# Optimization experiments

Hardware: AMD Instinct MI355X
Metric: run time of the kernel (lower is better)

## Reference

```python
import jax, jax.numpy as jnp
import numpy as np

D = 1024
H = 16
DH = D // H
FF = 4096
EPS = 1e-5


def _layernorm(x, g, b):
    m = jnp.mean(x, axis=-1, keepdims=True)
    v = jnp.mean(jnp.square(x - m), axis=-1, keepdims=True)
    return (x - m) * jax.lax.rsqrt(v + EPS) * g + b


def setup_inputs() -> dict:
    key = jax.random.key(0)
    ks = jax.random.split(key, 24)
    B, S = 2, 2048
    s = 0.02
    inp = {
        "tokens": jax.random.normal(ks[0], (B, S, D), jnp.float32),
        "attention_bias": jax.random.normal(ks[1], (B, S, S, 3), jnp.float32),
        "metadata_compatibility": jax.random.normal(ks[2], (B, S, S), jnp.float32),
        "key_padding_mask": jnp.zeros((B, S), jnp.bool_),
        "ln1_g": jnp.ones((D,), jnp.float32),
        "ln1_b": jnp.zeros((D,), jnp.float32),
        "Wq": jax.random.normal(ks[3], (D, D), jnp.float32) * s,
        "bq": jnp.zeros((D,), jnp.float32),
        "Wk": jax.random.normal(ks[4], (D, D), jnp.float32) * s,
        "bk": jnp.zeros((D,), jnp.float32),
        "Wv": jax.random.normal(ks[5], (D, D), jnp.float32) * s,
        "bv": jnp.zeros((D,), jnp.float32),
        "Wo": jax.random.normal(ks[6], (D, D), jnp.float32) * s,
        "bo": jnp.zeros((D,), jnp.float32),
        "Ws": jax.random.normal(ks[7], (3, H), jnp.float32) * s,
        "bs": jnp.zeros((H,), jnp.float32),
        "Wm": jax.random.normal(ks[8], (1, H), jnp.float32) * s,
        "bm": jnp.zeros((H,), jnp.float32),
        "ln2_g": jnp.ones((D,), jnp.float32),
        "ln2_b": jnp.zeros((D,), jnp.float32),
        "W1": jax.random.normal(ks[9], (D, FF), jnp.float32) * s,
        "b1": jnp.zeros((FF,), jnp.float32),
        "W2": jax.random.normal(ks[10], (FF, D), jnp.float32) * s,
        "b2": jnp.zeros((D,), jnp.float32),
    }
    return inp


def reference(tokens, attention_bias, metadata_compatibility, key_padding_mask,
              ln1_g, ln1_b, Wq, bq, Wk, bk, Wv, bv, Wo, bo,
              Ws, bs, Wm, bm, ln2_g, ln2_b, W1, b1, W2, b2):
    B, S, _ = tokens.shape
    scale = DH ** -0.5
    n = _layernorm(tokens, ln1_g, ln1_b)
    # project and split heads: [B,S,H,DH]
    q = (n @ Wq + bq).reshape(B, S, H, DH)
    k = (n @ Wk + bk).reshape(B, S, H, DH)
    v = (n @ Wv + bv).reshape(B, S, H, DH)
    logits = jnp.einsum('bihd,bjhd->bhij', q, k) * scale  # [B,H,S,S]
    # structural bias: Linear(3->H) then permute to [B,H,S,S]
    logits = logits + jnp.einsum('bijc,ch->bhij', attention_bias, Ws) + bs[None, :, None, None]
    # metadata bias: Linear(1->H)
    logits = logits + metadata_compatibility[:, None, :, :] * Wm[0][None, :, None, None] + bm[None, :, None, None]
    logits = jnp.where(key_padding_mask[:, None, None, :], -1e9, logits)
    w = jax.nn.softmax(logits, axis=-1)
    attended = jnp.einsum('bhij,bjhd->bihd', w, v).reshape(B, S, D)
    x = tokens + (attended @ Wo + bo)
    h = _layernorm(x, ln2_g, ln2_b)
    ff = jax.nn.gelu(h @ W1 + b1, approximate=False) @ W2 + b2
    return x + ff
```

## Files before the change

kernel.cpp:

```cpp
#include <hip/hip_runtime.h>

#define S_LEN 2048
#define DMODEL 1024
#define NH 16
#define DH 64
#define FFDIM 4096

typedef __bf16 bf16x8 __attribute__((ext_vector_type(8)));
typedef float f32x4 __attribute__((ext_vector_type(4)));
typedef unsigned short ushort_t;

#define AS1 __attribute__((address_space(1)))
#define AS3 __attribute__((address_space(3)))

__device__ __forceinline__ void gll16(const void* g, void* l) {
  __builtin_amdgcn_global_load_lds((AS1 const void*)g, (AS3 void*)l, 16, 0, 0);
}

__device__ __forceinline__ unsigned short f2b(float f){
  unsigned u = __builtin_bit_cast(unsigned, f);
  u = (u + 0x7FFFu + ((u >> 16) & 1u)) >> 16;
  return (unsigned short)u;
}

__device__ __forceinline__ float b2f(unsigned short us){
  return __builtin_bit_cast(float, (unsigned)us << 16);
}

__device__ __forceinline__ unsigned cvt_pk_bf16(float lo, float hi){
  unsigned r;
  asm("v_cvt_pk_bf16_f32 %0, %1, %2" : "=v"(r) : "v"(lo), "v"(hi));
  return r;
}

__device__ __forceinline__ float gelu_exact(float x){
  return 0.5f * x * (1.0f + erff(x * 0.70710678118654752f));
}

__device__ __forceinline__ f32x4 mfma16(bf16x8 a, bf16x8 b, f32x4 c){
  return __builtin_amdgcn_mfma_f32_16x16x32_bf16(a, b, c, 0, 0, 0);
}

__global__ __launch_bounds__(256) void tconv64(
    const float* __restrict__ s0, const float* __restrict__ s1,
    const float* __restrict__ s2, const float* __restrict__ s3,
    const float* __restrict__ s4, const float* __restrict__ s5,
    ushort_t* __restrict__ d0, ushort_t* __restrict__ d1,
    ushort_t* __restrict__ d2, ushort_t* __restrict__ d3,
    ushort_t* __restrict__ d4, ushort_t* __restrict__ d5)
{
  __shared__ float tile[64][65];
  int bx = blockIdx.x;
  const float* W; ushort_t* Wt; int K, N, n0, k0;
  if (bx < 1024) {
    int seg = bx >> 8, t_ = bx & 255;
    W  = (seg == 0) ? s0 : (seg == 1) ? s1 : (seg == 2) ? s2 : s3;
    Wt = (seg == 0) ? d0 : (seg == 1) ? d1 : (seg == 2) ? d2 : d3;
    K = 1024; N = 1024; n0 = (t_ & 15) * 64; k0 = (t_ >> 4) * 64;
  } else if (bx < 2048) {
    int t_ = bx - 1024;
    W = s4; Wt = d4; K = 1024; N = 4096;
    n0 = (t_ & 63) * 64; k0 = (t_ >> 6) * 64;
  } else {
    int t_ = bx - 2048;
    W = s5; Wt = d5; K = 4096; N = 1024;
    n0 = (t_ & 15) * 64; k0 = (t_ >> 4) * 64;
  }
  int t = threadIdx.x;
  int lrow = t >> 4, lcol = (t & 15) * 4;
#pragma unroll
  for (int i = 0; i < 4; ++i) {
    float4 v = *(const float4*)&W[(size_t)(k0 + lrow + i * 16) * N + n0 + lcol];
    tile[lrow + i * 16][lcol]     = v.x;
    tile[lrow + i * 16][lcol + 1] = v.y;
    tile[lrow + i * 16][lcol + 2] = v.z;
    tile[lrow + i * 16][lcol + 3] = v.w;
  }
  __syncthreads();
  int orow = t >> 2, oseg = (t & 3) * 16;
  alignas(16) ushort_t ob[16];
#pragma unroll
  for (int j = 0; j < 16; ++j) ob[j] = f2b(tile[oseg + j][orow]);
  *(uint4*)&Wt[(size_t)(n0 + orow) * K + k0 + oseg]     = *(const uint4*)ob;
  *(uint4*)&Wt[(size_t)(n0 + orow) * K + k0 + oseg + 8] = *((const uint4*)ob + 1);
}

__global__ __launch_bounds__(256) void ln_kernel(
    const float* __restrict__ x, const float* __restrict__ g,
    const float* __restrict__ bt, ushort_t* __restrict__ out)
{
  int row = blockIdx.x;
  int t = threadIdx.x;
  const float4 v = *(const float4*)&x[(size_t)row * DMODEL + t * 4];
  float s = v.x + v.y + v.z + v.w;
  float s2 = v.x*v.x + v.y*v.y + v.z*v.z + v.w*v.w;
#pragma unroll
  for (int d = 1; d < 64; d <<= 1) {
    s  += __shfl_xor(s,  d, 64);
    s2 += __shfl_xor(s2, d, 64);
  }
  __shared__ float red[8];
  int w = t >> 6;
  if ((t & 63) == 0) { red[w] = s; red[4 + w] = s2; }
  __syncthreads();
  s  = red[0] + red[1] + red[2] + red[3];
  s2 = red[4] + red[5] + red[6] + red[7];
  float mean = s * (1.0f / DMODEL);
  float var  = s2 * (1.0f / DMODEL) - mean * mean;
  float rstd = rsqrtf(var + 1e-5f);
  float4 gg = *(const float4*)&g[t * 4];
  float4 bb = *(const float4*)&bt[t * 4];
  ushort4 o;
  o.x = f2b((v.x - mean) * rstd * gg.x + bb.x);
  o.y = f2b((v.y - mean) * rstd * gg.y + bb.y);
  o.z = f2b((v.z - mean) * rstd * gg.z + bb.z);
  o.w = f2b((v.w - mean) * rstd * gg.w + bb.w);
  *(ushort4*)&out[(size_t)row * DMODEL + t * 4] = o;
}

__global__ __launch_bounds__(256) void bias_head_kernel(
    const float* __restrict__ ab, const float* __restrict__ mc,
    const unsigned char* __restrict__ kp,
    const float* __restrict__ Ws, const float* __restrict__ bs,
    const float* __restrict__ Wm, const float* __restrict__ bm,
    ushort_t* __restrict__ bp)
{
  int bi = blockIdx.x;
  int b = bi >> 11;
  int t = threadIdx.x;
  int j0 = t * 8;
  float av[24];
  const float4* A4 = (const float4*)(ab + ((size_t)bi * S_LEN + j0) * 3);
#pragma unroll
  for (int u = 0; u < 6; ++u) {
    float4 x = A4[u];
    av[u*4] = x.x; av[u*4+1] = x.y; av[u*4+2] = x.z; av[u*4+3] = x.w;
  }
  float mv[8];
  const float4* M4 = (const float4*)(mc + (size_t)bi * S_LEN + j0);
#pragma unroll
  for (int u = 0; u < 2; ++u) {
    float4 x = M4[u];
    mv[u*4] = x.x; mv[u*4+1] = x.y; mv[u*4+2] = x.z; mv[u*4+3] = x.w;
  }
  unsigned long long kq = *(const unsigned long long*)(kp + (size_t)b * S_LEN + j0);
#pragma unroll
  for (int h = 0; h < NH; ++h) {
    float w0 = Ws[h], w1 = Ws[NH + h], w2 = Ws[2*NH + h];
    float wm = Wm[h], cc = bs[h] + bm[h];
    float v[8];
#pragma unroll
    for (int j = 0; j < 8; ++j) {
      float vv = av[j*3]*w0 + av[j*3+1]*w1 + av[j*3+2]*w2 + mv[j]*wm + cc;
      if ((kq >> (8*j)) & 1ull) vv = -1e9f;
      v[j] = vv;
    }
    uint4 pk;
    pk.x = cvt_pk_bf16(v[0], v[1]);
    pk.y = cvt_pk_bf16(v[2], v[3]);
    pk.z = cvt_pk_bf16(v[4], v[5]);
    pk.w = cvt_pk_bf16(v[6], v[7]);
    *(uint4*)&bp[((size_t)(b*NH + h) * S_LEN + (bi & (S_LEN-1))) * S_LEN + j0] = pk;
  }
}

template<int MODE>
__global__ __launch_bounds__(256) void gemm_bt(
    const ushort_t* __restrict__ A, const ushort_t* __restrict__ Bt,
    const float* __restrict__ b0p, const float* __restrict__ b1p,
    const float* __restrict__ b2p,
    void* __restrict__ o0, void* __restrict__ o1, void* __restrict__ o2,
    int M, int N, int K)
{
  __shared__ ushort_t sh[2][8192];
  int t = threadIdx.x;
  int m0 = blockIdx.y * 128, n0 = blockIdx.x * 128;
  int w = t >> 6, l = t & 63, lr = l & 15, lg = l >> 4;
  int wr = (w >> 1) * 64, wc = (w & 1) * 64;

  const ushort_t* srcp[4];
  int dsto[4];
#pragma unroll
  for (int j = 0; j < 4; ++j) {
    int c = j * 4 + w;
    int o = c * 1024 + l * 16;
    if (c < 8)
      srcp[j] = &A[(size_t)(m0 + (o >> 6)) * K + ((o & 63) >> 1)];
    else {
      int o2 = o - 8192;
      srcp[j] = &Bt[(size_t)(n0 + (o2 >> 6)) * K + ((o2 & 63) >> 1)];
    }
    dsto[j] = o;
  }

#define GSTAGE(bi, kk) do { \
  _Pragma("unroll") \
  for (int j = 0; j < 4; ++j) gll16(srcp[j] + (kk), (char*)sh[bi] + dsto[j]); \
} while (0)

  GSTAGE(0, 0);
  __syncthreads();
  f32x4 acc[4][4] = {};
  int cur = 0;
  for (int k0 = 0; k0 < K; k0 += 32) {
    if (k0 + 32 < K) GSTAGE(cur ^ 1, k0 + 32);
    const ushort_t* s = sh[cur];
    bf16x8 af[4], bfr[4];
#pragma unroll
    for (int a = 0; a < 4; ++a)
      af[a] = *(const bf16x8*)&s[(wr + a * 16 + lr) * 32 + lg * 8];
#pragma unroll
    for (int b = 0; b < 4; ++b)
      bfr[b] = *(const bf16x8*)&s[4096 + (wc + b * 16 + lr) * 32 + lg * 8];
    __builtin_amdgcn_s_setprio(1);
#pragma unroll
    for (int a = 0; a < 4; ++a)
#pragma unroll
      for (int b = 0; b < 4; ++b)
        acc[a][b] = mfma16(af[a], bfr[b], acc[a][b]);
    __builtin_amdgcn_s_setprio(0);
    __syncthreads();
    cur ^= 1;
  }
#undef GSTAGE

  if (MODE == 3) {
    ushort_t* out = (ushort_t*)o0;
#pragma unroll
    for (int a = 0; a < 4; ++a)
#pragma unroll
      for (int b = 0; b < 4; ++b) {
        int gn = n0 + wc + b * 16 + lr;
        float bv = b0p[gn];
#pragma unroll
        for (int r = 0; r < 4; ++r) {
          int gm = m0 + wr + a * 16 + lg * 4 + r;
          out[(size_t)gm * N + gn] = f2b(gelu_exact(acc[a][b][r] + bv));
        }
      }
  } else {
    int seg = n0 >> 10;
    int nb0 = n0 & 1023;
    const float* bi = (seg == 0) ? b0p : (seg == 1) ? b1p : b2p;
    if (seg < 2) {
      ushort_t* out = (ushort_t*)((seg == 0) ? o0 : o1);
#pragma unroll
      for (int a = 0; a < 4; ++a)
#pragma unroll
        for (int b = 0; b < 4; ++b) {
          int nn = nb0 + wc + b * 16 + lr;
          float bv = bi[nn];
#pragma unroll
          for (int r = 0; r < 4; ++r) {
            int gm = m0 + wr + a * 16 + lg * 4 + r;
            out[(size_t)gm * DMODEL + nn] = f2b(acc[a][b][r] + bv);
          }
        }
    } else {
      ushort_t* out = (ushort_t*)o2;
#pragma unroll
      for (int a = 0; a < 4; ++a)
#pragma unroll
        for (int b = 0; b < 4; ++b) {
          int nn = nb0 + wc + b * 16 + lr;
          int gm = m0 + wr + a * 16 + lg * 4;
          float bv = bi[nn];
          ushort4 pk;
          pk.x = f2b(acc[a][b][0] + bv);
          pk.y = f2b(acc[a][b][1] + bv);
          pk.z = f2b(acc[a][b][2] + bv);
          pk.w = f2b(acc[a][b][3] + bv);
          size_t addr = (((size_t)(gm >> 11) * NH + (nn >> 6)) * DH + (nn & 63)) * S_LEN
                        + (gm & (S_LEN - 1));
          *(ushort4*)&out[addr] = pk;
        }
    }
  }
}

__global__ __launch_bounds__(256) void gemm64_res(
    const ushort_t* __restrict__ A, const ushort_t* __restrict__ Bt,
    const float* __restrict__ bias, const float* __restrict__ res,
    float* __restrict__ out, int M, int N, int K)
{
  __shared__ ushort_t sh[2][6144];
  int t = threadIdx.x;
  int m0 = blockIdx.y * 128, n0 = blockIdx.x * 64;
  int w = t >> 6, l = t & 63, lr = l & 15, lg = l >> 4;
  int wr = (w >> 1) * 64, wc = (w & 1) * 32;

  const ushort_t* srcp[3];
  int dsto[3];
#pragma unroll
  for (int j = 0; j < 3; ++j) {
    int c = j * 4 + w;
    int o = c * 1024 + l * 16;
    if (c < 8)
      srcp[j] = &A[(size_t)(m0 + (o >> 6)) * K + ((o & 63) >> 1)];
    else {
      int o2 = o - 8192;
      srcp[j] = &Bt[(size_t)(n0 + (o2 >> 6)) * K + ((o2 & 63) >> 1)];
    }
    dsto[j] = o;
  }

#define GSTAGE64(bi, kk) do { \
  _Pragma("unroll") \
  for (int j = 0; j < 3; ++j) gll16(srcp[j] + (kk), (char*)sh[bi] + dsto[j]); \
} while (0)

  GSTAGE64(0, 0);
  __syncthreads();
  f32x4 acc[4][2] = {};
  int cur = 0;
  for (int k0 = 0; k0 < K; k0 += 32) {
    if (k0 + 32 < K) GSTAGE64(cur ^ 1, k0 + 32);
    const ushort_t* s = sh[cur];
    bf16x8 af[4], bfr[2];
#pragma unroll
    for (int a = 0; a < 4; ++a)
      af[a] = *(const bf16x8*)&s[(wr + a * 16 + lr) * 32 + lg * 8];
#pragma unroll
    for (int b = 0; b < 2; ++b)
      bfr[b] = *(const bf16x8*)&s[4096 + (wc + b * 16 + lr) * 32 + lg * 8];
    __builtin_amdgcn_s_setprio(1);
#pragma unroll
    for (int a = 0; a < 4; ++a)
#pragma unroll
      for (int b = 0; b < 2; ++b)
        acc[a][b] = mfma16(af[a], bfr[b], acc[a][b]);
    __builtin_amdgcn_s_setprio(0);
    __syncthreads();
    cur ^= 1;
  }
#undef GSTAGE64

#pragma unroll
  for (int a = 0; a < 4; ++a)
#pragma unroll
    for (int b = 0; b < 2; ++b) {
      int gn = n0 + wc + b * 16 + lr;
      float bv = bias[gn];
#pragma unroll
      for (int r = 0; r < 4; ++r) {
        int gm = m0 + wr + a * 16 + lg * 4 + r;
        out[(size_t)gm * N + gn] = acc[a][b][r] + bv + res[(size_t)gm * N + gn];
      }
    }
}

__global__ __launch_bounds__(256) void attn_kernel(
    const ushort_t* __restrict__ q, const ushort_t* __restrict__ k,
    const ushort_t* __restrict__ vt, const ushort_t* __restrict__ bp,
    ushort_t* __restrict__ att)
{
  __shared__ ushort_t kbuf[2][4096];
  __shared__ ushort_t vbuf[2][4096];
  __shared__ ushort_t p_lds[4096];
  int bh = blockIdx.y;
  int b = bh >> 4, h = bh & 15;
  int i0 = blockIdx.x * 64;
  int t = threadIdx.x, w = t >> 6, l = t & 63;
  int lr = l & 15, lg = l >> 4;
  int rho = lr & 7;
  const float scale = 0.125f;
  const int NT = S_LEN / 64;

  int srow0 = t >> 3, srow1 = 32 + (t >> 3);
  int c16 = t & 7;
  size_t kb0 = (size_t)b * S_LEN * DMODEL + h * DH;
  size_t vb0 = (size_t)(b * NH + h) * DH * S_LEN;
  size_t koff0 = (size_t)srow0 * DMODEL + ((c16 ^ (srow0 & 7)) << 3);
  size_t koff1 = (size_t)srow1 * DMODEL + ((c16 ^ (srow1 & 7)) << 3);
  size_t voff0 = (size_t)srow0 * S_LEN + ((c16 ^ (srow0 & 7)) << 3);
  size_t voff1 = (size_t)srow1 * S_LEN + ((c16 ^ (srow1 & 7)) << 3);
  int do0 = t * 8, do1 = 2048 + t * 8;

#define STAGE_KV(bi, j0_) do { \
  size_t kr = kb0 + (size_t)(j0_) * DMODEL; \
  size_t vr = vb0 + (size_t)(j0_); \
  gll16(k + kr + koff0, &kbuf[bi][do0]); \
  gll16(k + kr + koff1, &kbuf[bi][do1]); \
  gll16(vt + vr + voff0, &vbuf[bi][do0]); \
  gll16(vt + vr + voff1, &vbuf[bi][do1]); \
} while (0)

  int qrow = i0 + w * 16 + lr;
  size_t qbase = (size_t)(b * S_LEN + qrow) * DMODEL + h * DH;
  bf16x8 aq0 = *(const bf16x8*)&q[qbase + lg * 8];
  bf16x8 aq1 = *(const bf16x8*)&q[qbase + 32 + lg * 8];

  const ushort_t* bprow = bp + ((size_t)bh * S_LEN + qrow) * S_LEN + lg * 4;

  f32x4 acc_o[4] = {};
  float m_run = -1e30f, l_run = 0.0f;

  uint2 braw[4];
#pragma unroll
  for (int n = 0; n < 4; ++n) braw[n] = *(const uint2*)(bprow + n * 16);

  STAGE_KV(0, 0);
  __syncthreads();

  for (int jt = 0; jt < NT; ++jt) {
    int cur = jt & 1;
    if (jt + 1 < NT) STAGE_KV(cur ^ 1, (jt + 1) * 64);

    uint2 bn[4] = {braw[0], braw[1], braw[2], braw[3]};
    if (jt + 1 < NT) {
      const ushort_t* bpt = bprow + (jt + 1) * 64;
#pragma unroll
      for (int n = 0; n < 4; ++n) bn[n] = *(const uint2*)(bpt + n * 16);
    }

    const char* kbc = (const char*)kbuf[cur];
    f32x4 acc_s[4] = {};
    __builtin_amdgcn_s_setprio(1);
#pragma unroll
    for (int n = 0; n < 4; ++n) {
      const char* rb = kbc + (n * 16 + lr) * 128;
      bf16x8 k0 = *(const bf16x8*)(rb + ((lg ^ rho) << 4));
      bf16x8 k1 = *(const bf16x8*)(rb + (((4 + lg) ^ rho) << 4));
      acc_s[n] = mfma16(k0, aq0, acc_s[n]);
      acc_s[n] = mfma16(k1, aq1, acc_s[n]);
    }
    __builtin_amdgcn_s_setprio(0);

    float p[16];
#pragma unroll
    for (int n = 0; n < 4; ++n) {
      p[n*4+0] = fmaf(acc_s[n][0], scale, b2f((unsigned short)(braw[n].x & 0xFFFF)));
      p[n*4+1] = fmaf(acc_s[n][1], scale, b2f((unsigned short)(braw[n].x >> 16)));
      p[n*4+2] = fmaf(acc_s[n][2], scale, b2f((unsigned short)(braw[n].y & 0xFFFF)));
      p[n*4+3] = fmaf(acc_s[n][3], scale, b2f((unsigned short)(braw[n].y >> 16)));
    }
    float t8[8], t4[4];
#pragma unroll
    for (int i = 0; i < 8; ++i) t8[i] = fmaxf(p[i], p[i + 8]);
#pragma unroll
    for (int i = 0; i < 4; ++i) t4[i] = fmaxf(t8[i], t8[i + 4]);
    float mx = fmaxf(fmaxf(t4[0], t4[1]), fmaxf(t4[2], t4[3]));
    mx = fmaxf(mx, __shfl_xor(mx, 16, 64));
    mx = fmaxf(mx, __shfl_xor(mx, 32, 64));

    if (!__all(mx <= m_run + 8.0f)) {
      float mnew = fmaxf(m_run, mx);
      float sf = __expf(m_run - mnew);
      m_run = mnew;
      l_run *= sf;
      float sfr[4];
#pragma unroll
      for (int r = 0; r < 4; ++r) sfr[r] = __shfl(sf, lg * 4 + r, 64);
#pragma unroll
      for (int nd = 0; nd < 4; ++nd)
#pragma unroll
        for (int r = 0; r < 4; ++r) acc_o[nd][r] *= sfr[r];
    }
#pragma unroll
    for (int i = 0; i < 16; ++i) p[i] = __expf(p[i] - m_run);
    float s8[8], s4[4];
#pragma unroll
    for (int i = 0; i < 8; ++i) s8[i] = p[i] + p[i + 8];
#pragma unroll
    for (int i = 0; i < 4; ++i) s4[i] = s8[i] + s8[i + 4];
    float ls = (s4[0] + s4[1]) + (s4[2] + s4[3]);
    ls += __shfl_xor(ls, 16, 64);
    ls += __shfl_xor(ls, 32, 64);
    l_run += ls;

    char* pb = (char*)p_lds + (w * 16 + lr) * 128;
#pragma unroll
    for (int n = 0; n < 4; ++n) {
      uint2 pk2;
      pk2.x = cvt_pk_bf16(p[n*4+0], p[n*4+1]);
      pk2.y = cvt_pk_bf16(p[n*4+2], p[n*4+3]);
      *(uint2*)(pb + ((n * 32 + lg * 8) ^ (rho << 4))) = pk2;
    }
    asm volatile("s_waitcnt lgkmcnt(0)" ::: "memory");
    __builtin_amdgcn_sched_barrier(0);

    bf16x8 ap0 = *(const bf16x8*)(pb + ((lg ^ rho) << 4));
    bf16x8 ap1 = *(const bf16x8*)(pb + (((4 + lg) ^ rho) << 4));
    const char* vbc = (const char*)vbuf[cur];
    __builtin_amdgcn_s_setprio(1);
#pragma unroll
    for (int nd = 0; nd < 4; ++nd) {
      const char* rb = vbc + (nd * 16 + lr) * 128;
      bf16x8 v0 = *(const bf16x8*)(rb + ((lg ^ rho) << 4));
      bf16x8 v1 = *(const bf16x8*)(rb + (((4 + lg) ^ rho) << 4));
      acc_o[nd] = mfma16(ap0, v0, acc_o[nd]);
      acc_o[nd] = mfma16(ap1, v1, acc_o[nd]);
    }
    __builtin_amdgcn_s_setprio(0);
    __syncthreads();
#pragma unroll
    for (int n = 0; n < 4; ++n) braw[n] = bn[n];
  }
#undef STAGE_KV

  float inv[4];
#pragma unroll
  for (int r = 0; r < 4; ++r) inv[r] = 1.0f / __shfl(l_run, lg * 4 + r, 64);
#pragma unroll
  for (int r = 0; r < 4; ++r) {
    int gr = i0 + w * 16 + lg * 4 + r;
#pragma unroll
    for (int nd = 0; nd < 4; ++nd)
      att[(size_t)(b * S_LEN + gr) * DMODEL + h * DH + nd * 16 + lr] =
          f2b(acc_o[nd][r] * inv[r]);
  }
}

extern "C" void kernel_launch(void* const* d_in, const int* in_sizes, int n_in,
                              void* d_out, int out_size, void* d_ws, size_t ws_size,
                              hipStream_t stream) {
  const float* tokens = (const float*)d_in[0];
  const float* ab     = (const float*)d_in[1];
  const float* mc     = (const float*)d_in[2];
  const unsigned char* kp = (const unsigned char*)d_in[3];
  const float* ln1g = (const float*)d_in[4];
  const float* ln1b = (const float*)d_in[5];
  const float* Wq = (const float*)d_in[6];
  const float* bq = (const float*)d_in[7];
  const float* Wk = (const float*)d_in[8];
  const float* bk = (const float*)d_in[9];
  const float* Wv = (const float*)d_in[10];
  const float* bv = (const float*)d_in[11];
  const float* Wo = (const float*)d_in[12];
  const float* bo = (const float*)d_in[13];
  const float* Ws = (const float*)d_in[14];
  const float* bs = (const float*)d_in[15];
  const float* Wm = (const float*)d_in[16];
  const float* bm = (const float*)d_in[17];
  const float* ln2g = (const float*)d_in[18];
  const float* ln2b = (const float*)d_in[19];
  const float* W1 = (const float*)d_in[20];
  const float* b1 = (const float*)d_in[21];
  const float* W2 = (const float*)d_in[22];
  const float* b2 = (const float*)d_in[23];
  float* out = (float*)d_out;

  int B = in_sizes[0] / (S_LEN * DMODEL);
  int M = B * S_LEN;

  char* ws = (char*)d_ws;
  ushort_t* nb  = (ushort_t*)(ws + 0);
  ushort_t* qb  = (ushort_t*)(ws + (size_t)8388608);
  ushort_t* kb  = (ushort_t*)(ws + (size_t)16777216);
  ushort_t* vtb = (ushort_t*)(ws + (size_t)25165824);
  ushort_t* ff1 = (ushort_t*)(ws + 0);
  ushort_t* wt_q = (ushort_t*)(ws + (size_t)33554432);
  ushort_t* wt_k = (ushort_t*)(ws + (size_t)35651584);
  ushort_t* wt_v = (ushort_t*)(ws + (size_t)37748736);
  ushort_t* wt_o = (ushort_t*)(ws + (size_t)39845888);
  ushort_t* wt_1 = (ushort_t*)(ws + (size_t)41943040);
  ushort_t* wt_2 = (ushort_t*)(ws + (size_t)50331648);
  ushort_t* attb = (ushort_t*)(ws + (size_t)58720256);
  float*    xb   = (float*)   (ws + (size_t)67108864);
  ushort_t* hb   = (ushort_t*)(ws + (size_t)83886080);
  ushort_t* bp   = (ushort_t*)(ws + (size_t)92274688);

  tconv64<<<3072, 256, 0, stream>>>(Wq, Wk, Wv, Wo, W1, W2,
                                    wt_q, wt_k, wt_v, wt_o, wt_1, wt_2);

  ln_kernel<<<M, 256, 0, stream>>>(tokens, ln1g, ln1b, nb);

  bias_head_kernel<<<M, 256, 0, stream>>>(ab, mc, kp, Ws, bs, Wm, bm, bp);

  gemm_bt<4><<<dim3(24, M / 128), 256, 0, stream>>>(
      nb, wt_q, bq, bk, bv, qb, kb, vtb, M, 3 * DMODEL, DMODEL);

  attn_kernel<<<dim3(S_LEN / 64, B * NH), 256, 0, stream>>>(qb, kb, vtb, bp, attb);

  gemm64_res<<<dim3(16, M / 128), 256, 0, stream>>>(
      attb, wt_o, bo, tokens, xb, M, DMODEL, DMODEL);

  ln_kernel<<<M, 256, 0, stream>>>(xb, ln2g, ln2b, hb);

  gemm_bt<3><<<dim3(32, M / 128), 256, 0, stream>>>(
      hb, wt_1, b1, nullptr, nullptr, ff1, nullptr, nullptr, M, FFDIM, DMODEL);

  gemm64_res<<<dim3(16, M / 128), 256, 0, stream>>>(
      ff1, wt_2, b2, xb, out, M, DMODEL, FFDIM);
}
```

Measured before the change: 636.4 us.

## Keep softmax probabilities in registers via permlane swaps and use exp2 domain

The attention kernel no longer round-trips the bf16 probability tile through LDS to reshape it from the QK^T accumulator layout into the PV MFMA A-operand layout. It uses v_permlane32/16_swap instructions to do the reshuffle in registers. Scores are moved into base-2 by folding log2(e) into the scale and into the precomputed bias, so exp2f replaces __expf, and the lazy-rescale threshold is adjusted to match. The row-sum reduction is moved after the PV MFMAs to overlap with them. The risk is that the permlane mapping must exactly match the layout the LDS path produced.

```diff
diff --git a/kernel.cpp b/kernel.cpp
--- a/kernel.cpp
+++ b/kernel.cpp
@@ -5,9 +5,11 @@
 #define NH 16
 #define DH 64
 #define FFDIM 4096
+#define L2E 1.4426950408889634f
 
 typedef __bf16 bf16x8 __attribute__((ext_vector_type(8)));
 typedef float f32x4 __attribute__((ext_vector_type(4)));
+typedef unsigned u32x4 __attribute__((ext_vector_type(4)));
 typedef unsigned short ushort_t;
 
 #define AS1 __attribute__((address_space(1)))
@@ -31,6 +33,13 @@
   unsigned r;
   asm("v_cvt_pk_bf16_f32 %0, %1, %2" : "=v"(r) : "v"(lo), "v"(hi));
   return r;
+}
+
+__device__ __forceinline__ void plane_swap32(unsigned &a, unsigned &b){
+  asm volatile("v_permlane32_swap_b32 %0, %1" : "+v"(a), "+v"(b));
+}
+__device__ __forceinline__ void plane_swap16(unsigned &a, unsigned &b){
+  asm volatile("v_permlane16_swap_b32 %0, %1" : "+v"(a), "+v"(b));
 }
 
 __device__ __forceinline__ float gelu_exact(float x){
@@ -146,13 +155,13 @@
   unsigned long long kq = *(const unsigned long long*)(kp + (size_t)b * S_LEN + j0);
 #pragma unroll
   for (int h = 0; h < NH; ++h) {
-    float w0 = Ws[h], w1 = Ws[NH + h], w2 = Ws[2*NH + h];
-    float wm = Wm[h], cc = bs[h] + bm[h];
+    float w0 = Ws[h] * L2E, w1 = Ws[NH + h] * L2E, w2 = Ws[2*NH + h] * L2E;
+    float wm = Wm[h] * L2E, cc = (bs[h] + bm[h]) * L2E;
     float v[8];
 #pragma unroll
     for (int j = 0; j < 8; ++j) {
       float vv = av[j*3]*w0 + av[j*3+1]*w1 + av[j*3+2]*w2 + mv[j]*wm + cc;
-      if ((kq >> (8*j)) & 1ull) vv = -1e9f;
+      if ((kq >> (8*j)) & 1ull) vv = -2e9f;
       v[j] = vv;
     }
     uint4 pk;
@@ -356,14 +365,13 @@
 {
   __shared__ ushort_t kbuf[2][4096];
   __shared__ ushort_t vbuf[2][4096];
-  __shared__ ushort_t p_lds[4096];
   int bh = blockIdx.y;
   int b = bh >> 4, h = bh & 15;
   int i0 = blockIdx.x * 64;
   int t = threadIdx.x, w = t >> 6, l = t & 63;
   int lr = l & 15, lg = l >> 4;
   int rho = lr & 7;
-  const float scale = 0.125f;
+  const float scale = 0.125f * L2E;
   const int NT = S_LEN / 64;
 
   int srow0 = t >> 3, srow1 = 32 + (t >> 3);
@@ -443,9 +451,9 @@
     mx = fmaxf(mx, __shfl_xor(mx, 16, 64));
     mx = fmaxf(mx, __shfl_xor(mx, 32, 64));
 
-    if (!__all(mx <= m_run + 8.0f)) {
+    if (!__all(mx <= m_run + 11.6f)) {
       float mnew = fmaxf(m_run, mx);
-      float sf = __expf(m_run - mnew);
+      float sf = exp2f(m_run - mnew);
       m_run = mnew;
       l_run *= sf;
       float sfr[4];
@@ -457,30 +465,25 @@
         for (int r = 0; r < 4; ++r) acc_o[nd][r] *= sfr[r];
     }
 #pragma unroll
-    for (int i = 0; i < 16; ++i) p[i] = __expf(p[i] - m_run);
-    float s8[8], s4[4];
-#pragma unroll
-    for (int i = 0; i < 8; ++i) s8[i] = p[i] + p[i + 8];
-#pragma unroll
-    for (int i = 0; i < 4; ++i) s4[i] = s8[i] + s8[i + 4];
-    float ls = (s4[0] + s4[1]) + (s4[2] + s4[3]);
-    ls += __shfl_xor(ls, 16, 64);
-    ls += __shfl_xor(ls, 32, 64);
-    l_run += ls;
-
-    char* pb = (char*)p_lds + (w * 16 + lr) * 128;
-#pragma unroll
-    for (int n = 0; n < 4; ++n) {
-      uint2 pk2;
-      pk2.x = cvt_pk_bf16(p[n*4+0], p[n*4+1]);
-      pk2.y = cvt_pk_bf16(p[n*4+2], p[n*4+3]);
-      *(uint2*)(pb + ((n * 32 + lg * 8) ^ (rho << 4))) = pk2;
-    }
-    asm volatile("s_waitcnt lgkmcnt(0)" ::: "memory");
-    __builtin_amdgcn_sched_barrier(0);
-
-    bf16x8 ap0 = *(const bf16x8*)(pb + ((lg ^ rho) << 4));
-    bf16x8 ap1 = *(const bf16x8*)(pb + (((4 + lg) ^ rho) << 4));
+    for (int i = 0; i < 16; ++i) p[i] = exp2f(p[i] - m_run);
+
+    unsigned c00 = cvt_pk_bf16(p[0],  p[1]);
+    unsigned c01 = cvt_pk_bf16(p[2],  p[3]);
+    unsigned c10 = cvt_pk_bf16(p[4],  p[5]);
+    unsigned c11 = cvt_pk_bf16(p[6],  p[7]);
+    unsigned c20 = cvt_pk_bf16(p[8],  p[9]);
+    unsigned c21 = cvt_pk_bf16(p[10], p[11]);
+    unsigned c30 = cvt_pk_bf16(p[12], p[13]);
+    unsigned c31 = cvt_pk_bf16(p[14], p[15]);
+    plane_swap32(c00, c10); plane_swap16(c00, c10);
+    plane_swap32(c01, c11); plane_swap16(c01, c11);
+    plane_swap32(c20, c30); plane_swap16(c20, c30);
+    plane_swap32(c21, c31); plane_swap16(c21, c31);
+    u32x4 av0 = {c00, c01, c10, c11};
+    u32x4 av1 = {c20, c21, c30, c31};
+    bf16x8 ap0 = __builtin_bit_cast(bf16x8, av0);
+    bf16x8 ap1 = __builtin_bit_cast(bf16x8, av1);
+
     const char* vbc = (const char*)vbuf[cur];
     __builtin_amdgcn_s_setprio(1);
 #pragma unroll
@@ -492,6 +495,17 @@
       acc_o[nd] = mfma16(ap1, v1, acc_o[nd]);
     }
     __builtin_amdgcn_s_setprio(0);
+
+    float s8[8], s4[4];
+#pragma unroll
+    for (int i = 0; i < 8; ++i) s8[i] = p[i] + p[i + 8];
+#pragma unroll
+    for (int i = 0; i < 4; ++i) s4[i] = s8[i] + s8[i + 4];
+    float ls = (s4[0] + s4[1]) + (s4[2] + s4[3]);
+    ls += __shfl_xor(ls, 16, 64);
+    ls += __shfl_xor(ls, 32, 64);
+    l_run += ls;
+
     __syncthreads();
 #pragma unroll
     for (int n = 0; n < 4; ++n) braw[n] = bn[n];
```

Result: no change. 644.5 us (+1.3%).
